# Optimization experiments

Measured on AMD Instinct MI355X. Metric: run time of the kernel, lower is better.

Reference implementation:

```python
import jax, jax.numpy as jnp
import numpy as np

N, E = 50000, 800000
NODE_IN, EDGE_IN = 32, 16
EMB, GEMB = 128, 128
H, C, L, B = 4, 32, 2, 8   # heads, per-head dim, layers, graphs
GAT_IN = NODE_IN + EMB      # skip_conn=True
NEG_SLOPE = 0.2
EPS = 1e-5


def layernorm(x, g, b):
    m = jnp.mean(x, -1, keepdims=True)
    v = jnp.mean((x - m) ** 2, -1, keepdims=True)
    return (x - m) / jnp.sqrt(v + EPS) * g + b


def setup_inputs() -> dict:
    key = jax.random.key(0)
    ks = jax.random.split(key, 24)
    s = 0.05
    return {
        "x": jax.random.normal(ks[0], (N, NODE_IN), jnp.float32),
        "edge_attr": jax.random.normal(ks[1], (E, EDGE_IN), jnp.float32),
        "W_in": jax.random.normal(ks[2], (NODE_IN, EMB), jnp.float32) * s,
        "b_in": jnp.zeros((EMB,), jnp.float32),
        "W_src": jax.random.normal(ks[3], (L, GAT_IN, H * C), jnp.float32) * s,
        "W_edge": jax.random.normal(ks[4], (L, EDGE_IN, H * C), jnp.float32) * s,
        "att_src": jax.random.normal(ks[5], (L, H, C), jnp.float32) * s,
        "att_dst": jax.random.normal(ks[6], (L, H, C), jnp.float32) * s,
        "att_edge": jax.random.normal(ks[7], (L, H, C), jnp.float32) * s,
        "gat_bias": jnp.zeros((L, H * C), jnp.float32),
        "ln_gamma": jnp.ones((L, EMB), jnp.float32),
        "ln_beta": jnp.zeros((L, EMB), jnp.float32),
        "W_out": jax.random.normal(ks[8], (EMB, EMB), jnp.float32) * s,
        "b_out": jnp.zeros((EMB,), jnp.float32),
        "ln_out_gamma": jnp.ones((EMB,), jnp.float32),
        "ln_out_beta": jnp.zeros((EMB,), jnp.float32),
        "W_g": jax.random.normal(ks[9], (EMB, GEMB), jnp.float32) * s,
        "b_g": jnp.zeros((GEMB,), jnp.float32),
        "g_gamma": jnp.ones((GEMB,), jnp.float32),
        "g_beta": jnp.zeros((GEMB,), jnp.float32),
        "edge_index": jax.random.randint(ks[10], (2, E), 0, N, jnp.int32),
        "batch": jnp.sort(jax.random.randint(ks[11], (N,), 0, B, jnp.int32)),
    }


def reference(x, edge_attr, W_in, b_in, W_src, W_edge, att_src, att_dst, att_edge,
              gat_bias, ln_gamma, ln_beta, W_out, b_out, ln_out_gamma, ln_out_beta,
              W_g, b_g, g_gamma, g_beta, edge_index, batch):
    # PyG GATConv adds self-loops with edge_attr fill_value='mean'
    loop = jnp.arange(N, dtype=edge_index.dtype)
    src = jnp.concatenate([edge_index[0], loop])   # [E2]
    dst = jnp.concatenate([edge_index[1], loop])   # [E2]
    ea = jnp.concatenate([edge_attr, jnp.broadcast_to(edge_attr.mean(0), (N, EDGE_IN))], 0)

    h = jax.nn.relu(x @ W_in + b_in)  # [N, EMB]
    for l in range(L):
        inp = jnp.concatenate([x, h], -1)                   # skip connection [N, GAT_IN]
        xs = (inp @ W_src[l]).reshape(N, H, C)              # projected nodes
        a_s = jnp.einsum('nhc,hc->nh', xs, att_src[l])
        a_d = jnp.einsum('nhc,hc->nh', xs, att_dst[l])
        ee = (ea @ W_edge[l]).reshape(-1, H, C)             # [E2, H, C]
        a_e = jnp.einsum('ehc,hc->eh', ee, att_edge[l])
        alpha = jax.nn.leaky_relu(a_s[src] + a_d[dst] + a_e, NEG_SLOPE)  # [E2, H]
        # segment softmax over incoming edges of each destination node
        amax = jax.ops.segment_max(alpha, dst, num_segments=N)
        ex = jnp.exp(alpha - amax[dst])
        denom = jax.ops.segment_sum(ex, dst, num_segments=N)
        w = ex / (denom[dst] + 1e-16)
        msg = xs[src] * w[:, :, None]                        # [E2, H, C]
        out = jax.ops.segment_sum(msg, dst, num_segments=N).reshape(N, H * C) + gat_bias[l]
        h = jax.nn.elu(layernorm(out, ln_gamma[l], ln_beta[l]))

    g = layernorm(jax.nn.relu(h @ W_g + b_g), g_gamma, g_beta)
    gsum = jax.ops.segment_sum(g, batch, num_segments=B)
    cnt = jax.ops.segment_sum(jnp.ones((N, 1), g.dtype), batch, num_segments=B)
    graph_embeddings = gsum / jnp.maximum(cnt, 1.0)

    node_embeddings = layernorm(jax.nn.relu(h @ W_out + b_out), ln_out_gamma, ln_out_beta)
    return node_embeddings, graph_embeddings
```

## Files before the change

### kernel.cpp

```cpp
#include <hip/hip_runtime.h>

#define N_NODES 50000
#define N_EDGES 800000
#define E2      850000
#define NODE_IN 32
#define EDGE_IN 16
#define EMB     128
#define GAT_IN  160
#define NLAYER  2
#define NGRAPH  8
#define NBLK    196
#define NB32    1563
#define NB64    782
#define EB      3321

#define GWT_SRC0 0
#define GWT_SRC1 20480
#define GWT_OUT  40960
#define GWT_G    57344
#define GWT_TOT  73728

typedef short bf16x8 __attribute__((ext_vector_type(8)));
typedef float f32x4 __attribute__((ext_vector_type(4)));

__device__ __forceinline__ unsigned int f2bf(float f) {
    unsigned int u = __float_as_uint(f);
    return (u + 0x7FFFu + ((u >> 16) & 1u)) >> 16;
}
__device__ __forceinline__ float bf2f(unsigned int h) {
    return __uint_as_float(h << 16);
}
__device__ __forceinline__ unsigned int pack2bf(float a, float b) {
    return f2bf(a) | (f2bf(b) << 16);
}

__global__ void zero_kernel(float* __restrict__ p, int n) {
    int i = blockIdx.x * blockDim.x + threadIdx.x;
    int stride = gridDim.x * blockDim.x;
    for (; i < n; i += stride) p[i] = 0.f;
}

__global__ __launch_bounds__(256) void mega_kernel(
    const int* __restrict__ edge_index, const float* __restrict__ edge_attr,
    const float* __restrict__ x, const float* __restrict__ W_in,
    const float* __restrict__ b_in,
    const float* __restrict__ Wsrc, const float* __restrict__ Wout,
    const float* __restrict__ Wg,
    int* __restrict__ cnt8, int* __restrict__ rank, float* __restrict__ meta,
    unsigned int* __restrict__ h_bf, unsigned int* __restrict__ x_bf,
    unsigned short* __restrict__ gwt) {
    __shared__ float smem[32 * NODE_IN];
    int b = blockIdx.x, t = threadIdx.x;

    if (b < EB) {
        int e = b * 256 + t;
        if (e < E2) {
            int dst = (e < N_EDGES) ? edge_index[N_EDGES + e] : (e - N_EDGES);
            int shard = b & 7;
            rank[e] = atomicAdd(&cnt8[shard * N_NODES + dst], 1);
        }
        if (b < 512) {
            if (t < 16) smem[t] = 0.f;
            __syncthreads();
            int gid = b * 256 + t;
            int q = gid & 3;
            const float4* ea4 = (const float4*)edge_attr;
            float4 s = make_float4(0.f, 0.f, 0.f, 0.f);
            for (int j = gid; j < N_EDGES * 4; j += 512 * 256) {
                float4 v = ea4[j];
                s.x += v.x; s.y += v.y; s.z += v.z; s.w += v.w;
            }
            atomicAdd(&smem[q * 4 + 0], s.x);
            atomicAdd(&smem[q * 4 + 1], s.y);
            atomicAdd(&smem[q * 4 + 2], s.z);
            atomicAdd(&smem[q * 4 + 3], s.w);
            __syncthreads();
            if (t < 16) atomicAdd(&meta[t], smem[t]);
        }
    } else if (b < EB + NB32) {
        float (*inp)[NODE_IN] = (float (*)[NODE_IN])smem;
        int n0 = (b - EB) * 32;
        for (int i = t; i < 32 * NODE_IN; i += 256) {
            int r = i >> 5, c = i & 31;
            int n = min(n0 + r, N_NODES - 1);
            inp[r][c] = x[(size_t)n * NODE_IN + c];
        }
        __syncthreads();
        for (int i = t; i < 32 * 16; i += 256) {
            int r = i >> 4, c = i & 15;
            int n = n0 + r;
            if (n < N_NODES) x_bf[(size_t)n * 16 + c] = pack2bf(inp[r][2 * c], inp[r][2 * c + 1]);
        }
        int wave = t >> 6, lane = t & 63;
        int c0 = lane * 2, c1 = c0 + 1;
        const float2* W2 = (const float2*)W_in;
        float acc[8][2];
#pragma unroll
        for (int j = 0; j < 8; j++) { acc[j][0] = b_in[c0]; acc[j][1] = b_in[c1]; }
#pragma unroll 2
        for (int k4 = 0; k4 < NODE_IN / 4; k4++) {
            float4 v[8];
#pragma unroll
            for (int j = 0; j < 8; j++) v[j] = *(const float4*)&inp[wave * 8 + j][k4 * 4];
#pragma unroll
            for (int kk = 0; kk < 4; kk++) {
                float2 w = W2[(k4 * 4 + kk) * 64 + lane];
#pragma unroll
                for (int j = 0; j < 8; j++) {
                    float vv = (&v[j].x)[kk];
                    acc[j][0] += vv * w.x;
                    acc[j][1] += vv * w.y;
                }
            }
        }
#pragma unroll
        for (int j = 0; j < 8; j++) {
            int n = n0 + wave * 8 + j;
            if (n < N_NODES)
                h_bf[(size_t)n * 64 + lane] = pack2bf(fmaxf(acc[j][0], 0.f), fmaxf(acc[j][1], 0.f));
        }
    } else {
        int g = (b - EB - NB32) * 256 + t;
        const float* Wm;
        int base, gg;
        if (g < 5120) {
            int l = g / 2560;
            gg = g - l * 2560;
            Wm = Wsrc + (size_t)l * GAT_IN * EMB;
            base = l * 20480;
        } else if (g < 7168) {
            gg = g - 5120;
            Wm = Wout;
            base = GWT_OUT;
        } else {
            gg = g - 7168;
            Wm = Wg;
            base = GWT_G;
        }
        int lane = gg & 63, tmp = gg >> 6;
        int nt = tmp & 7, kc = tmp >> 3;
        int quad = lane >> 4, l16 = lane & 15;
        int col = nt * 16 + l16, k0 = kc * 32 + quad * 8;
        unsigned int u[4];
#pragma unroll
        for (int j = 0; j < 4; j++)
            u[j] = pack2bf(Wm[(size_t)(k0 + 2 * j) * EMB + col],
                           Wm[(size_t)(k0 + 2 * j + 1) * EMB + col]);
        *(uint4*)(gwt + base + (size_t)gg * 8) = make_uint4(u[0], u[1], u[2], u[3]);
    }
}

__global__ __launch_bounds__(256) void scan1_kernel(const int* __restrict__ cnt8,
                                                    int* __restrict__ bsum) {
    __shared__ int sm[256];
    int t = threadIdx.x;
    int i = blockIdx.x * 256 + t;
    int tot = 0;
    if (i < N_NODES) {
#pragma unroll
        for (int s = 0; s < 8; s++) tot += cnt8[s * N_NODES + i];
    }
    sm[t] = tot;
    __syncthreads();
#pragma unroll
    for (int d = 128; d >= 1; d >>= 1) {
        if (t < d) sm[t] += sm[t + d];
        __syncthreads();
    }
    if (t == 0) bsum[blockIdx.x] = sm[0];
}

__global__ __launch_bounds__(256) void scan2_prep_kernel(const int* __restrict__ bsum,
                                                         int* __restrict__ bbase,
                                                         const float* __restrict__ W_edge,
                                                         const float* __restrict__ att_edge,
                                                         float* __restrict__ meta) {
    __shared__ int sm[256];
    int t = threadIdx.x;
    int v = (t < NBLK) ? bsum[t] : 0;
    sm[t] = v;
    __syncthreads();
#pragma unroll
    for (int d = 1; d < 256; d <<= 1) {
        int u = (t >= d) ? sm[t - d] : 0;
        __syncthreads();
        sm[t] += u;
        __syncthreads();
    }
    if (t < NBLK) bbase[t] = sm[t] - v;

    if (t < EDGE_IN) meta[t] = meta[t] * (1.0f / (float)N_EDGES);
    __syncthreads();
    if (t < 128) {
        int l = t >> 6, k = (t >> 2) & 15, h = t & 3;
        const float* w = W_edge + ((size_t)l * EDGE_IN + k) * EMB + h * 32;
        const float* a = att_edge + (size_t)l * EMB + h * 32;
        float acc = 0.f;
#pragma unroll
        for (int c = 0; c < 32; c++) acc += w[c] * a[c];
        meta[16 + (l * 16 + k) * 4 + h] = acc;
    }
    __syncthreads();
    if (t < 8) {
        int l = t >> 2, h = t & 3;
        float acc = 0.f;
#pragma unroll
        for (int k = 0; k < EDGE_IN; k++) acc += meta[k] * meta[16 + (l * 16 + k) * 4 + h];
        meta[144 + t] = acc;
    }
}

__global__ __launch_bounds__(256) void scan3_kernel(const int* __restrict__ bbase,
                                                    const int* __restrict__ cnt8,
                                                    int* __restrict__ off,
                                                    int* __restrict__ shard_base) {
    __shared__ int sm[256];
    int t = threadIdx.x;
    int i = blockIdx.x * 256 + t;
    int c[8] = {0, 0, 0, 0, 0, 0, 0, 0};
    int tot = 0;
    if (i < N_NODES) {
#pragma unroll
        for (int s = 0; s < 8; s++) {
            c[s] = cnt8[s * N_NODES + i];
            tot += c[s];
        }
    }
    sm[t] = tot;
    __syncthreads();
#pragma unroll
    for (int d = 1; d < 256; d <<= 1) {
        int u = (t >= d) ? sm[t - d] : 0;
        __syncthreads();
        sm[t] += u;
        __syncthreads();
    }
    if (i < N_NODES) {
        int base = bbase[blockIdx.x] + sm[t] - tot;
        off[i] = base;
        int4 sb0, sb1;
        sb0.x = base;           base += c[0];
        sb0.y = base;           base += c[1];
        sb0.z = base;           base += c[2];
        sb0.w = base;           base += c[3];
        sb1.x = base;           base += c[4];
        sb1.y = base;           base += c[5];
        sb1.z = base;           base += c[6];
        sb1.w = base;
        *(int4*)(shard_base + (size_t)i * 8) = sb0;
        *(int4*)(shard_base + (size_t)i * 8 + 4) = sb1;
        if (i == N_NODES - 1) off[N_NODES] = E2;
    }
}

__global__ __launch_bounds__(256) void fill_perm_kernel(const int* __restrict__ edge_index,
                                                        const int* __restrict__ rank,
                                                        const int* __restrict__ shard_base,
                                                        int* __restrict__ perm) {
    int e = blockIdx.x * 256 + threadIdx.x;
    if (e >= E2) return;
    int src, dst;
    if (e < N_EDGES) {
        src = edge_index[e];
        dst = edge_index[N_EDGES + e];
    } else {
        src = dst = e - N_EDGES;
    }
    int shard = (e >> 8) & 7;
    int pos = shard_base[(size_t)dst * 8 + shard] + rank[e];
    ((int2*)perm)[pos] = make_int2(src, e);
}

__global__ __launch_bounds__(256) void compute_ae_kernel(const int* __restrict__ perm,
                                                         const float* __restrict__ edge_attr,
                                                         const float* __restrict__ meta,
                                                         int* __restrict__ csr_src,
                                                         float* __restrict__ csr_ae0,
                                                         float* __restrict__ csr_ae1) {
    __shared__ float Ml[128];
    __shared__ float loop_ae[8];
    int t = threadIdx.x;
    if (t < 128) Ml[t] = meta[16 + t];
    if (t < 8) loop_ae[t] = meta[144 + t];
    __syncthreads();
    int p = blockIdx.x * 256 + t;
    if (p >= E2) return;
    int2 pe = ((const int2*)perm)[p];
    int src = pe.x, e = pe.y;
    csr_src[p] = src;
    float ae[2][4];
    if (e < N_EDGES) {
        const float4* r4 = (const float4*)(edge_attr + (size_t)e * EDGE_IN);
#pragma unroll
        for (int l = 0; l < 2; l++)
#pragma unroll
            for (int hh = 0; hh < 4; hh++) ae[l][hh] = 0.f;
#pragma unroll
        for (int q = 0; q < 4; q++) {
            float4 v = r4[q];
#pragma unroll
            for (int l = 0; l < 2; l++) {
                const float* M = Ml + l * 64;
#pragma unroll
                for (int hh = 0; hh < 4; hh++) {
                    ae[l][hh] += v.x * M[(4 * q + 0) * 4 + hh] + v.y * M[(4 * q + 1) * 4 + hh] +
                                 v.z * M[(4 * q + 2) * 4 + hh] + v.w * M[(4 * q + 3) * 4 + hh];
                }
            }
        }
    } else {
#pragma unroll
        for (int l = 0; l < 2; l++)
#pragma unroll
            for (int hh = 0; hh < 4; hh++) ae[l][hh] = loop_ae[l * 4 + hh];
    }
    *(float4*)(csr_ae0 + (size_t)p * 4) = make_float4(ae[0][0], ae[0][1], ae[0][2], ae[0][3]);
    *(float4*)(csr_ae1 + (size_t)p * 4) = make_float4(ae[1][0], ae[1][1], ae[1][2], ae[1][3]);
}

template <int K, int MODE>
__global__ __launch_bounds__(256) void dense_mfma_kernel(
    const unsigned int* __restrict__ xbf, const unsigned int* __restrict__ hbf,
    const unsigned short* __restrict__ gwt, const float* __restrict__ bias,
    const float* __restrict__ v1, const float* __restrict__ v2,
    const int* __restrict__ batch,
    unsigned int* __restrict__ xs_out, float* __restrict__ a_s, float* __restrict__ a_d,
    float* __restrict__ out_nodes, float* __restrict__ gsum, float* __restrict__ gcnt) {
    constexpr int CLS = 132;
    __shared__ __align__(16) float cl[64 * CLS];
    __shared__ float red[(MODE != 0) ? 64 : 1][8];
    __shared__ float locw[(MODE == 2) ? 4 : 1][2][EMB];
    __shared__ int bids[(MODE == 2) ? 64 : 1];

    int t = threadIdx.x;
    int n0 = blockIdx.x * 64;
    if (MODE == 2 && t < 64) bids[t] = batch[min(n0 + t, N_NODES - 1)];

    int wave = t >> 6, lane = t & 63;
    int quad = lane >> 4, l16 = lane & 15;
    int arow = min(n0 + wave * 16 + l16, N_NODES - 1);
    const bf16x8* B = (const bf16x8*)gwt;
    f32x4 acc[8];
#pragma unroll
    for (int i = 0; i < 8; i++) acc[i] = (f32x4){0.f, 0.f, 0.f, 0.f};
#pragma unroll
    for (int kc = 0; kc < K / 32; kc++) {
        bf16x8 af;
        if (MODE == 0 && kc == 0) {
            af = *(const bf16x8*)(xbf + (size_t)arow * 16 + quad * 4);
        } else {
            int hk = ((MODE == 0) ? (kc - 1) : kc) * 16;
            af = *(const bf16x8*)(hbf + (size_t)arow * 64 + hk + quad * 4);
        }
#pragma unroll
        for (int nt = 0; nt < 8; nt++) {
            bf16x8 bfv = B[(kc * 8 + nt) * 64 + lane];
            acc[nt] = __builtin_amdgcn_mfma_f32_16x16x32_bf16(af, bfv, acc[nt], 0, 0, 0);
        }
    }
#pragma unroll
    for (int nt = 0; nt < 8; nt++) {
#pragma unroll
        for (int i = 0; i < 4; i++) {
            int r = wave * 16 + quad * 4 + i;
            cl[r * CLS + nt * 16 + l16] = acc[nt][i];
        }
    }
    __syncthreads();

    int p = t & 3, r = t >> 2;
    int n = n0 + r;
    const float4* c4 = (const float4*)(cl + r * CLS + p * 32);

    if (MODE == 0) {
        const float4* s4 = (const float4*)(v1 + p * 32);
        const float4* d4 = (const float4*)(v2 + p * 32);
        if (n < N_NODES) {
            float s_ = 0.f, d_ = 0.f;
#pragma unroll
            for (int i = 0; i < 8; i++) {
                float4 cv = c4[i], sv = s4[i], dv = d4[i];
                s_ += cv.x * sv.x + cv.y * sv.y + cv.z * sv.z + cv.w * sv.w;
                d_ += cv.x * dv.x + cv.y * dv.y + cv.z * dv.z + cv.w * dv.w;
                uint2 pk = make_uint2(pack2bf(cv.x, cv.y), pack2bf(cv.z, cv.w));
                *(uint2*)(xs_out + (size_t)n * 64 + p * 16 + 2 * i) = pk;
            }
            a_s[(size_t)n * 4 + p] = s_;
            a_d[(size_t)n * 4 + p] = d_;
        }
    } else {
        const float4* b4 = (const float4*)(bias + p * 32);
        float vals[32];
        float s_ = 0.f, q_ = 0.f;
#pragma unroll
        for (int i = 0; i < 8; i++) {
            float4 cv = c4[i], bv = b4[i];
            float w0 = fmaxf(cv.x + bv.x, 0.f), w1 = fmaxf(cv.y + bv.y, 0.f);
            float w2 = fmaxf(cv.z + bv.z, 0.f), w3 = fmaxf(cv.w + bv.w, 0.f);
            vals[4 * i] = w0; vals[4 * i + 1] = w1; vals[4 * i + 2] = w2; vals[4 * i + 3] = w3;
            s_ += w0 + w1 + w2 + w3;
            q_ += w0 * w0 + w1 * w1 + w2 * w2 + w3 * w3;
        }
        red[r][p] = s_;
        red[r][4 + p] = q_;
        __syncthreads();
        float sm = red[r][0] + red[r][1] + red[r][2] + red[r][3];
        float sq = red[r][4] + red[r][5] + red[r][6] + red[r][7];
        float mean = sm * (1.f / EMB);
        float var = sq * (1.f / EMB) - mean * mean;
        float rstd = rsqrtf(var + 1e-5f);
        const float4* g4 = (const float4*)(v1 + p * 32);
        const float4* be4 = (const float4*)(v2 + p * 32);
#pragma unroll
        for (int i = 0; i < 8; i++) {
            float4 gv = g4[i], bv = be4[i];
            vals[4 * i]     = (vals[4 * i]     - mean) * rstd * gv.x + bv.x;
            vals[4 * i + 1] = (vals[4 * i + 1] - mean) * rstd * gv.y + bv.y;
            vals[4 * i + 2] = (vals[4 * i + 2] - mean) * rstd * gv.z + bv.z;
            vals[4 * i + 3] = (vals[4 * i + 3] - mean) * rstd * gv.w + bv.w;
        }
        if (MODE == 1) {
            if (n < N_NODES) {
                float* op = out_nodes + (size_t)n * EMB + p * 32;
#pragma unroll
                for (int i = 0; i < 8; i++)
                    *(float4*)(op + 4 * i) = make_float4(vals[4 * i], vals[4 * i + 1],
                                                         vals[4 * i + 2], vals[4 * i + 3]);
            }
        } else {
            int nvalid = min(64, N_NODES - n0);
            int bmin = bids[0], bmax = bids[nvalid - 1];
            int bid = bids[r];
            bool inA = (bid == bmin) && (n < N_NODES);
            bool inB = (bid == bmax) && (bmax != bmin) && (n < N_NODES);
            if (n < N_NODES && bid != bmin && bid != bmax) {
#pragma unroll
                for (int i = 0; i < 32; i++)
                    atomicAdd(&gsum[(size_t)bid * EMB + p * 32 + i], vals[i]);
            }
#pragma unroll
            for (int g = 0; g < 2; g++) {
                bool m = g ? inB : inA;
#pragma unroll
                for (int i = 0; i < 32; i++) {
                    float v = m ? vals[i] : 0.f;
                    v += __shfl_xor(v, 4, 64);
                    v += __shfl_xor(v, 8, 64);
                    v += __shfl_xor(v, 16, 64);
                    v += __shfl_xor(v, 32, 64);
                    if ((lane >> 2) == 0) locw[wave][g][(lane & 3) * 32 + i] = v;
                }
            }
            __syncthreads();
            if (t < 128) {
                float sA = locw[0][0][t] + locw[1][0][t] + locw[2][0][t] + locw[3][0][t];
                atomicAdd(&gsum[(size_t)bmin * EMB + t], sA);
                if (bmax != bmin) {
                    float sB = locw[0][1][t] + locw[1][1][t] + locw[2][1][t] + locw[3][1][t];
                    atomicAdd(&gsum[(size_t)bmax * EMB + t], sB);
                }
            } else if (t == 255) {
                int cA = 0, cB = 0;
                for (int rr = 0; rr < nvalid; rr++) {
                    int bb = bids[rr];
                    if (bb == bmin) cA++;
                    else if (bb == bmax) cB++;
                    else atomicAdd(&gcnt[bb], 1.f);
                }
                atomicAdd(&gcnt[bmin], (float)cA);
                if (bmax != bmin && cB > 0) atomicAdd(&gcnt[bmax], (float)cB);
            }
        }
    }
}

__global__ __launch_bounds__(256) void gat_gather_kernel(const int* __restrict__ off,
                                                         const int* __restrict__ csr_src,
                                                         const float* __restrict__ csr_ae,
                                                         const unsigned int* __restrict__ xs,
                                                         const float* __restrict__ a_s,
                                                         const float* __restrict__ a_d,
                                                         const float* __restrict__ bias_l,
                                                         const float* __restrict__ gamma_l,
                                                         const float* __restrict__ beta_l,
                                                         unsigned int* __restrict__ h_bf) {
    int t = threadIdx.x, wave = t >> 6, lane = t & 63;
    int n = blockIdx.x * 4 + wave;
    int g = lane >> 4, l16 = lane & 15;
    int h = l16 >> 2;
    float ad = a_d[(size_t)n * 4 + h];
    int p0 = __builtin_amdgcn_readfirstlane(off[n]);
    int p1 = __builtin_amdgcn_readfirstlane(off[n + 1]);
    int plast = p1 - 1;
    float den = 0.f;
    float acc[8];
#pragma unroll
    for (int j = 0; j < 8; j++) acc[j] = 0.f;

    for (int pb = p0; pb < p1; pb += 8) {
        int pA = pb + g, pB = pb + 4 + g;
        int iA = min(pA, plast), iB = min(pB, plast);
        int sA = csr_src[iA], sB = csr_src[iB];
        float aeA = csr_ae[(size_t)iA * 4 + h];
        float aeB = csr_ae[(size_t)iB * 4 + h];
        float asA = a_s[(size_t)sA * 4 + h];
        float asB = a_s[(size_t)sB * 4 + h];
        uint4 xA = *(const uint4*)(xs + (size_t)sA * 64 + l16 * 4);
        uint4 xB = *(const uint4*)(xs + (size_t)sB * 64 + l16 * 4);
        float alA = asA + ad + aeA;
        alA = alA > 0.f ? alA : 0.2f * alA;
        float exA = (pA <= plast) ? __expf(alA) : 0.f;
        float alB = asB + ad + aeB;
        alB = alB > 0.f ? alB : 0.2f * alB;
        float exB = (pB <= plast) ? __expf(alB) : 0.f;
        den += exA + exB;
        unsigned int u;
        u = xA.x; acc[0] += exA * bf2f(u & 0xFFFFu); acc[1] += exA * bf2f(u >> 16);
        u = xA.y; acc[2] += exA * bf2f(u & 0xFFFFu); acc[3] += exA * bf2f(u >> 16);
        u = xA.z; acc[4] += exA * bf2f(u & 0xFFFFu); acc[5] += exA * bf2f(u >> 16);
        u = xA.w; acc[6] += exA * bf2f(u & 0xFFFFu); acc[7] += exA * bf2f(u >> 16);
        u = xB.x; acc[0] += exB * bf2f(u & 0xFFFFu); acc[1] += exB * bf2f(u >> 16);
        u = xB.y; acc[2] += exB * bf2f(u & 0xFFFFu); acc[3] += exB * bf2f(u >> 16);
        u = xB.z; acc[4] += exB * bf2f(u & 0xFFFFu); acc[5] += exB * bf2f(u >> 16);
        u = xB.w; acc[6] += exB * bf2f(u & 0xFFFFu); acc[7] += exB * bf2f(u >> 16);
    }
#pragma unroll
    for (int j = 0; j < 8; j++) {
        acc[j] += __shfl_xor(acc[j], 16, 64);
        acc[j] += __shfl_xor(acc[j], 32, 64);
    }
    den += __shfl_xor(den, 16, 64);
    den += __shfl_xor(den, 32, 64);

    float dinv = 1.0f / (den + 1e-16f);
    int c0 = l16 * 8;
    const float4* b4 = (const float4*)(bias_l + c0);
    float4 bv0 = b4[0], bv1 = b4[1];
    float v[8];
    v[0] = acc[0] * dinv + bv0.x; v[1] = acc[1] * dinv + bv0.y;
    v[2] = acc[2] * dinv + bv0.z; v[3] = acc[3] * dinv + bv0.w;
    v[4] = acc[4] * dinv + bv1.x; v[5] = acc[5] * dinv + bv1.y;
    v[6] = acc[6] * dinv + bv1.z; v[7] = acc[7] * dinv + bv1.w;
    float sm = 0.f, sq = 0.f;
#pragma unroll
    for (int j = 0; j < 8; j++) { sm += v[j]; sq += v[j] * v[j]; }
#pragma unroll
    for (int o = 1; o <= 8; o <<= 1) {
        sm += __shfl_xor(sm, o, 64);
        sq += __shfl_xor(sq, o, 64);
    }
    float mean = sm * (1.f / EMB);
    float var = sq * (1.f / EMB) - mean * mean;
    float rstd = rsqrtf(var + 1e-5f);
    const float4* g4 = (const float4*)(gamma_l + c0);
    const float4* be4 = (const float4*)(beta_l + c0);
    float4 gv0 = g4[0], gv1 = g4[1], bev0 = be4[0], bev1 = be4[1];
    float y[8];
    y[0] = (v[0] - mean) * rstd * gv0.x + bev0.x;
    y[1] = (v[1] - mean) * rstd * gv0.y + bev0.y;
    y[2] = (v[2] - mean) * rstd * gv0.z + bev0.z;
    y[3] = (v[3] - mean) * rstd * gv0.w + bev0.w;
    y[4] = (v[4] - mean) * rstd * gv1.x + bev1.x;
    y[5] = (v[5] - mean) * rstd * gv1.y + bev1.y;
    y[6] = (v[6] - mean) * rstd * gv1.z + bev1.z;
    y[7] = (v[7] - mean) * rstd * gv1.w + bev1.w;
#pragma unroll
    for (int j = 0; j < 8; j++) y[j] = y[j] > 0.f ? y[j] : __expf(y[j]) - 1.f;
    if (g == 0) {
        uint4 o4;
        o4.x = pack2bf(y[0], y[1]);
        o4.y = pack2bf(y[2], y[3]);
        o4.z = pack2bf(y[4], y[5]);
        o4.w = pack2bf(y[6], y[7]);
        *(uint4*)(h_bf + (size_t)n * 64 + l16 * 4) = o4;
    }
}

__global__ void graph_out_kernel(const float* __restrict__ gsum, const float* __restrict__ gcnt,
                                 float* __restrict__ out) {
    int i = blockIdx.x * blockDim.x + threadIdx.x;
    if (i >= NGRAPH * EMB) return;
    int b = i >> 7;
    float c = fmaxf(gcnt[b], 1.f);
    out[(size_t)N_NODES * EMB + i] = gsum[i] / c;
}

extern "C" void kernel_launch(void* const* d_in, const int* in_sizes, int n_in,
                              void* d_out, int out_size, void* d_ws, size_t ws_size,
                              hipStream_t stream) {
    (void)in_sizes; (void)n_in; (void)out_size; (void)ws_size;
    const float* x         = (const float*)d_in[0];
    const float* edge_attr = (const float*)d_in[1];
    const float* W_in      = (const float*)d_in[2];
    const float* b_in      = (const float*)d_in[3];
    const float* W_src     = (const float*)d_in[4];
    const float* W_edge    = (const float*)d_in[5];
    const float* att_src   = (const float*)d_in[6];
    const float* att_dst   = (const float*)d_in[7];
    const float* att_edge  = (const float*)d_in[8];
    const float* gat_bias  = (const float*)d_in[9];
    const float* ln_gamma  = (const float*)d_in[10];
    const float* ln_beta   = (const float*)d_in[11];
    const float* W_out     = (const float*)d_in[12];
    const float* b_out     = (const float*)d_in[13];
    const float* ln_og     = (const float*)d_in[14];
    const float* ln_ob     = (const float*)d_in[15];
    const float* W_g       = (const float*)d_in[16];
    const float* b_g       = (const float*)d_in[17];
    const float* g_gamma   = (const float*)d_in[18];
    const float* g_beta    = (const float*)d_in[19];
    const int* edge_index  = (const int*)d_in[20];
    const int* batch       = (const int*)d_in[21];
    float* out = (float*)d_out;

    float* ws              = (float*)d_ws;
    unsigned int* h_bf     = (unsigned int*)ws;
    unsigned int* xs       = h_bf + (size_t)N_NODES * 64;
    unsigned int* x_bf     = xs + (size_t)N_NODES * 64;
    float* a_s             = (float*)(x_bf + (size_t)N_NODES * 16);
    float* a_d             = a_s + (size_t)N_NODES * 4;
    float* csr_ae          = a_d + (size_t)N_NODES * 4;
    unsigned short* gwt    = (unsigned short*)(csr_ae + (size_t)2 * E2 * 4);
    float* meta            = (float*)(gwt + GWT_TOT);
    float* gsum            = meta + 152;
    float* gcnt            = gsum + NGRAPH * EMB;
    int*   cnt8            = (int*)(gcnt + NGRAPH);
    int*   off             = cnt8 + 8 * N_NODES;
    int*   shard_base      = off + N_NODES + 1;
    int*   rank            = shard_base + 8 * N_NODES;
    int*   csr_src         = rank + E2;
    int*   bsum            = csr_src + E2;
    int*   bbase           = bsum + NBLK;
    int*   perm            = (int*)xs;

    zero_kernel<<<256, 256, 0, stream>>>(meta, 152 + NGRAPH * EMB + NGRAPH + 8 * N_NODES);
    mega_kernel<<<EB + NB32 + 36, 256, 0, stream>>>(
        edge_index, edge_attr, x, W_in, b_in, W_src, W_out, W_g,
        cnt8, rank, meta, h_bf, x_bf, gwt);

    scan1_kernel<<<NBLK, 256, 0, stream>>>(cnt8, bsum);
    scan2_prep_kernel<<<1, 256, 0, stream>>>(bsum, bbase, W_edge, att_edge, meta);
    scan3_kernel<<<NBLK, 256, 0, stream>>>(bbase, cnt8, off, shard_base);
    fill_perm_kernel<<<EB, 256, 0, stream>>>(edge_index, rank, shard_base, perm);
    compute_ae_kernel<<<EB, 256, 0, stream>>>(perm, edge_attr, meta,
                                              csr_src, csr_ae, csr_ae + (size_t)E2 * 4);

    for (int l = 0; l < NLAYER; l++) {
        dense_mfma_kernel<GAT_IN, 0><<<NB64, 256, 0, stream>>>(
            x_bf, h_bf, gwt + (l ? GWT_SRC1 : GWT_SRC0), nullptr,
            att_src + (size_t)l * EMB, att_dst + (size_t)l * EMB, nullptr,
            xs, a_s, a_d, nullptr, nullptr, nullptr);
        gat_gather_kernel<<<N_NODES / 4, 256, 0, stream>>>(
            off, csr_src, csr_ae + (size_t)l * E2 * 4, xs, a_s, a_d,
            gat_bias + (size_t)l * EMB, ln_gamma + (size_t)l * EMB,
            ln_beta + (size_t)l * EMB, h_bf);
    }

    dense_mfma_kernel<EMB, 1><<<NB64, 256, 0, stream>>>(
        nullptr, h_bf, gwt + GWT_OUT, b_out, ln_og, ln_ob, nullptr,
        nullptr, nullptr, nullptr, out, nullptr, nullptr);
    dense_mfma_kernel<EMB, 2><<<NB64, 256, 0, stream>>>(
        nullptr, h_bf, gwt + GWT_G, b_g, g_gamma, g_beta, batch,
        nullptr, nullptr, nullptr, nullptr, gsum, gcnt);
    graph_out_kernel<<<4, 256, 0, stream>>>(gsum, gcnt, out);
}
```

Measured before the change: 421.8 us.

## Replace sharded atomic CSR build with two-level bucket counting sort

Replaces the CSR construction, which used per-node sharded global atomic counters, a three-pass scan and a rank-based scatter, with a two-level counting sort. Edges are first histogrammed into 98 buckets of 512 destinations per 4096-edge chunk using shared-memory atomics, then scattered into bucket order. Each bucket is then sorted locally in shared memory to produce the offsets and the permutation. This removes the large zeroing of 400K counters and the contended global atomics, but adds an extra pass over the edge records. Only 98 blocks run the local sort, which limits parallelism, and the ordering within each node may differ from before.

```diff
diff --git a/kernel.cpp b/kernel.cpp
--- a/kernel.cpp
+++ b/kernel.cpp
@@ -9,10 +9,13 @@
 #define GAT_IN  160
 #define NLAYER  2
 #define NGRAPH  8
-#define NBLK    196
 #define NB32    1563
 #define NB64    782
 #define EB      3321
+
+#define NBUCK   98
+#define CHUNK   4096
+#define NCHUNK  208
 
 #define GWT_SRC0 0
 #define GWT_SRC1 20480
@@ -46,40 +49,47 @@
     const float* __restrict__ b_in,
     const float* __restrict__ Wsrc, const float* __restrict__ Wout,
     const float* __restrict__ Wg,
-    int* __restrict__ cnt8, int* __restrict__ rank, float* __restrict__ meta,
+    int* __restrict__ hist, float* __restrict__ meta,
     unsigned int* __restrict__ h_bf, unsigned int* __restrict__ x_bf,
     unsigned short* __restrict__ gwt) {
     __shared__ float smem[32 * NODE_IN];
     int b = blockIdx.x, t = threadIdx.x;
 
-    if (b < EB) {
-        int e = b * 256 + t;
-        if (e < E2) {
-            int dst = (e < N_EDGES) ? edge_index[N_EDGES + e] : (e - N_EDGES);
-            int shard = b & 7;
-            rank[e] = atomicAdd(&cnt8[shard * N_NODES + dst], 1);
-        }
-        if (b < 512) {
-            if (t < 16) smem[t] = 0.f;
-            __syncthreads();
-            int gid = b * 256 + t;
-            int q = gid & 3;
-            const float4* ea4 = (const float4*)edge_attr;
-            float4 s = make_float4(0.f, 0.f, 0.f, 0.f);
-            for (int j = gid; j < N_EDGES * 4; j += 512 * 256) {
-                float4 v = ea4[j];
-                s.x += v.x; s.y += v.y; s.z += v.z; s.w += v.w;
-            }
-            atomicAdd(&smem[q * 4 + 0], s.x);
-            atomicAdd(&smem[q * 4 + 1], s.y);
-            atomicAdd(&smem[q * 4 + 2], s.z);
-            atomicAdd(&smem[q * 4 + 3], s.w);
-            __syncthreads();
-            if (t < 16) atomicAdd(&meta[t], smem[t]);
-        }
-    } else if (b < EB + NB32) {
+    if (b < NCHUNK) {
+        int* lh = (int*)smem;
+        if (t < NBUCK) lh[t] = 0;
+        __syncthreads();
+        int c0 = b * CHUNK;
+#pragma unroll
+        for (int i = 0; i < CHUNK / 256; i++) {
+            int e = c0 + i * 256 + t;
+            if (e < E2) {
+                int dst = (e < N_EDGES) ? edge_index[N_EDGES + e] : (e - N_EDGES);
+                atomicAdd(&lh[dst >> 9], 1);
+            }
+        }
+        __syncthreads();
+        if (t < NBUCK) hist[t * NCHUNK + b] = lh[t];
+    } else if (b < NCHUNK + 512) {
+        if (t < 16) smem[t] = 0.f;
+        __syncthreads();
+        int gid = (b - NCHUNK) * 256 + t;
+        int q = gid & 3;
+        const float4* ea4 = (const float4*)edge_attr;
+        float4 s = make_float4(0.f, 0.f, 0.f, 0.f);
+        for (int j = gid; j < N_EDGES * 4; j += 512 * 256) {
+            float4 v = ea4[j];
+            s.x += v.x; s.y += v.y; s.z += v.z; s.w += v.w;
+        }
+        atomicAdd(&smem[q * 4 + 0], s.x);
+        atomicAdd(&smem[q * 4 + 1], s.y);
+        atomicAdd(&smem[q * 4 + 2], s.z);
+        atomicAdd(&smem[q * 4 + 3], s.w);
+        __syncthreads();
+        if (t < 16) atomicAdd(&meta[t], smem[t]);
+    } else if (b < NCHUNK + 512 + NB32) {
         float (*inp)[NODE_IN] = (float (*)[NODE_IN])smem;
-        int n0 = (b - EB) * 32;
+        int n0 = (b - NCHUNK - 512) * 32;
         for (int i = t; i < 32 * NODE_IN; i += 256) {
             int r = i >> 5, c = i & 31;
             int n = min(n0 + r, N_NODES - 1);
@@ -120,7 +130,7 @@
                 h_bf[(size_t)n * 64 + lane] = pack2bf(fmaxf(acc[j][0], 0.f), fmaxf(acc[j][1], 0.f));
         }
     } else {
-        int g = (b - EB - NB32) * 256 + t;
+        int g = (b - NCHUNK - 512 - NB32) * 256 + t;
         const float* Wm;
         int base, gg;
         if (g < 5120) {
@@ -150,34 +160,32 @@
     }
 }
 
-__global__ __launch_bounds__(256) void scan1_kernel(const int* __restrict__ cnt8,
-                                                    int* __restrict__ bsum) {
+__global__ __launch_bounds__(256) void bucket_scan_kernel(int* __restrict__ hist,
+                                                          int* __restrict__ btot) {
+    __shared__ int sm[256];
+    int k = blockIdx.x, t = threadIdx.x;
+    int v = (t < NCHUNK) ? hist[k * NCHUNK + t] : 0;
+    sm[t] = v;
+    __syncthreads();
+#pragma unroll
+    for (int d = 1; d < 256; d <<= 1) {
+        int u = (t >= d) ? sm[t - d] : 0;
+        __syncthreads();
+        sm[t] += u;
+        __syncthreads();
+    }
+    if (t < NCHUNK) hist[k * NCHUNK + t] = sm[t] - v;
+    if (t == 255) btot[k] = sm[255];
+}
+
+__global__ __launch_bounds__(256) void base_prep_kernel(const int* __restrict__ btot,
+                                                        int* __restrict__ bucket_base,
+                                                        const float* __restrict__ W_edge,
+                                                        const float* __restrict__ att_edge,
+                                                        float* __restrict__ meta) {
     __shared__ int sm[256];
     int t = threadIdx.x;
-    int i = blockIdx.x * 256 + t;
-    int tot = 0;
-    if (i < N_NODES) {
-#pragma unroll
-        for (int s = 0; s < 8; s++) tot += cnt8[s * N_NODES + i];
-    }
-    sm[t] = tot;
-    __syncthreads();
-#pragma unroll
-    for (int d = 128; d >= 1; d >>= 1) {
-        if (t < d) sm[t] += sm[t + d];
-        __syncthreads();
-    }
-    if (t == 0) bsum[blockIdx.x] = sm[0];
-}
-
-__global__ __launch_bounds__(256) void scan2_prep_kernel(const int* __restrict__ bsum,
-                                                         int* __restrict__ bbase,
-                                                         const float* __restrict__ W_edge,
-                                                         const float* __restrict__ att_edge,
-                                                         float* __restrict__ meta) {
-    __shared__ int sm[256];
-    int t = threadIdx.x;
-    int v = (t < NBLK) ? bsum[t] : 0;
+    int v = (t < NBUCK) ? btot[t] : 0;
     sm[t] = v;
     __syncthreads();
 #pragma unroll
@@ -187,7 +195,8 @@
         sm[t] += u;
         __syncthreads();
     }
-    if (t < NBLK) bbase[t] = sm[t] - v;
+    if (t < NBUCK) bucket_base[t] = sm[t] - v;
+    if (t == NBUCK - 1) bucket_base[NBUCK] = sm[t];
 
     if (t < EDGE_IN) meta[t] = meta[t] * (1.0f / (float)N_EDGES);
     __syncthreads();
@@ -210,68 +219,72 @@
     }
 }
 
-__global__ __launch_bounds__(256) void scan3_kernel(const int* __restrict__ bbase,
-                                                    const int* __restrict__ cnt8,
-                                                    int* __restrict__ off,
-                                                    int* __restrict__ shard_base) {
-    __shared__ int sm[256];
-    int t = threadIdx.x;
-    int i = blockIdx.x * 256 + t;
-    int c[8] = {0, 0, 0, 0, 0, 0, 0, 0};
-    int tot = 0;
-    if (i < N_NODES) {
-#pragma unroll
-        for (int s = 0; s < 8; s++) {
-            c[s] = cnt8[s * N_NODES + i];
-            tot += c[s];
-        }
-    }
-    sm[t] = tot;
-    __syncthreads();
-#pragma unroll
-    for (int d = 1; d < 256; d <<= 1) {
+__global__ __launch_bounds__(256) void scatter_bucket_kernel(const int* __restrict__ edge_index,
+                                                             const int* __restrict__ hist,
+                                                             const int* __restrict__ bucket_base,
+                                                             int2* __restrict__ brec) {
+    __shared__ int cur[NBUCK];
+    int b = blockIdx.x, t = threadIdx.x;
+    if (t < NBUCK) cur[t] = bucket_base[t] + hist[t * NCHUNK + b];
+    __syncthreads();
+    int c0 = b * CHUNK;
+#pragma unroll
+    for (int i = 0; i < CHUNK / 256; i++) {
+        int e = c0 + i * 256 + t;
+        if (e < E2) {
+            int src, dst;
+            if (e < N_EDGES) {
+                src = edge_index[e];
+                dst = edge_index[N_EDGES + e];
+            } else {
+                src = dst = e - N_EDGES;
+            }
+            int pos = atomicAdd(&cur[dst >> 9], 1);
+            brec[pos] = make_int2(src | ((dst & 511) << 16), e);
+        }
+    }
+}
+
+__global__ __launch_bounds__(512) void local_sort_kernel(const int* __restrict__ bucket_base,
+                                                         const int2* __restrict__ brec,
+                                                         int* __restrict__ off,
+                                                         int2* __restrict__ perm) {
+    __shared__ int lh[512];
+    __shared__ int sm[512];
+    int k = blockIdx.x, t = threadIdx.x;
+    int base = bucket_base[k], end = bucket_base[k + 1], cnt = end - base;
+    lh[t] = 0;
+    __syncthreads();
+    for (int i = t; i < cnt; i += 512) {
+        int2 r = brec[base + i];
+        atomicAdd(&lh[(r.x >> 16) & 511], 1);
+    }
+    __syncthreads();
+    int v = lh[t];
+    sm[t] = v;
+    __syncthreads();
+#pragma unroll
+    for (int d = 1; d < 512; d <<= 1) {
         int u = (t >= d) ? sm[t - d] : 0;
         __syncthreads();
         sm[t] += u;
         __syncthreads();
     }
-    if (i < N_NODES) {
-        int base = bbase[blockIdx.x] + sm[t] - tot;
-        off[i] = base;
-        int4 sb0, sb1;
-        sb0.x = base;           base += c[0];
-        sb0.y = base;           base += c[1];
-        sb0.z = base;           base += c[2];
-        sb0.w = base;           base += c[3];
-        sb1.x = base;           base += c[4];
-        sb1.y = base;           base += c[5];
-        sb1.z = base;           base += c[6];
-        sb1.w = base;
-        *(int4*)(shard_base + (size_t)i * 8) = sb0;
-        *(int4*)(shard_base + (size_t)i * 8 + 4) = sb1;
-        if (i == N_NODES - 1) off[N_NODES] = E2;
-    }
-}
-
-__global__ __launch_bounds__(256) void fill_perm_kernel(const int* __restrict__ edge_index,
-                                                        const int* __restrict__ rank,
-                                                        const int* __restrict__ shard_base,
-                                                        int* __restrict__ perm) {
-    int e = blockIdx.x * 256 + threadIdx.x;
-    if (e >= E2) return;
-    int src, dst;
-    if (e < N_EDGES) {
-        src = edge_index[e];
-        dst = edge_index[N_EDGES + e];
-    } else {
-        src = dst = e - N_EDGES;
-    }
-    int shard = (e >> 8) & 7;
-    int pos = shard_base[(size_t)dst * 8 + shard] + rank[e];
-    ((int2*)perm)[pos] = make_int2(src, e);
-}
-
-__global__ __launch_bounds__(256) void compute_ae_kernel(const int* __restrict__ perm,
+    int excl = sm[t] - v;
+    int dst = (k << 9) + t;
+    if (dst < N_NODES) off[dst] = base + excl;
+    if (k == NBUCK - 1 && t == 0) off[N_NODES] = E2;
+    lh[t] = excl;
+    __syncthreads();
+    for (int i = t; i < cnt; i += 512) {
+        int2 r = brec[base + i];
+        int dl = (r.x >> 16) & 511;
+        int p = atomicAdd(&lh[dl], 1);
+        perm[base + p] = make_int2(r.x & 0xFFFF, r.y);
+    }
+}
+
+__global__ __launch_bounds__(256) void compute_ae_kernel(const int2* __restrict__ perm,
                                                          const float* __restrict__ edge_attr,
                                                          const float* __restrict__ meta,
                                                          int* __restrict__ csr_src,
@@ -285,7 +298,7 @@
     __syncthreads();
     int p = blockIdx.x * 256 + t;
     if (p >= E2) return;
-    int2 pe = ((const int2*)perm)[p];
+    int2 pe = perm[p];
     int src = pe.x, e = pe.y;
     csr_src[p] = src;
     float ae[2][4];
@@ -624,24 +637,23 @@
     float* meta            = (float*)(gwt + GWT_TOT);
     float* gsum            = meta + 152;
     float* gcnt            = gsum + NGRAPH * EMB;
-    int*   cnt8            = (int*)(gcnt + NGRAPH);
-    int*   off             = cnt8 + 8 * N_NODES;
-    int*   shard_base      = off + N_NODES + 1;
-    int*   rank            = shard_base + 8 * N_NODES;
-    int*   csr_src         = rank + E2;
-    int*   bsum            = csr_src + E2;
-    int*   bbase           = bsum + NBLK;
-    int*   perm            = (int*)xs;
-
-    zero_kernel<<<256, 256, 0, stream>>>(meta, 152 + NGRAPH * EMB + NGRAPH + 8 * N_NODES);
-    mega_kernel<<<EB + NB32 + 36, 256, 0, stream>>>(
+    int*   off             = (int*)(gcnt + NGRAPH);
+    int*   csr_src         = off + N_NODES + 2;
+    int2*  brec            = (int2*)(csr_src + E2);
+    int*   hist            = (int*)(brec + E2);
+    int*   btot            = hist + NBUCK * NCHUNK;
+    int*   bucket_base     = btot + NBUCK;
+    int2*  perm            = (int2*)xs;
+
+    zero_kernel<<<8, 256, 0, stream>>>(meta, 152 + NGRAPH * EMB + NGRAPH);
+    mega_kernel<<<NCHUNK + 512 + NB32 + 36, 256, 0, stream>>>(
         edge_index, edge_attr, x, W_in, b_in, W_src, W_out, W_g,
-        cnt8, rank, meta, h_bf, x_bf, gwt);
-
-    scan1_kernel<<<NBLK, 256, 0, stream>>>(cnt8, bsum);
-    scan2_prep_kernel<<<1, 256, 0, stream>>>(bsum, bbase, W_edge, att_edge, meta);
-    scan3_kernel<<<NBLK, 256, 0, stream>>>(bbase, cnt8, off, shard_base);
-    fill_perm_kernel<<<EB, 256, 0, stream>>>(edge_index, rank, shard_base, perm);
+        hist, meta, h_bf, x_bf, gwt);
+
+    bucket_scan_kernel<<<NBUCK, 256, 0, stream>>>(hist, btot);
+    base_prep_kernel<<<1, 256, 0, stream>>>(btot, bucket_base, W_edge, att_edge, meta);
+    scatter_bucket_kernel<<<NCHUNK, 256, 0, stream>>>(edge_index, hist, bucket_base, brec);
+    local_sort_kernel<<<NBUCK, 512, 0, stream>>>(bucket_base, brec, off, perm);
     compute_ae_kernel<<<EB, 256, 0, stream>>>(perm, edge_attr, meta,
                                               csr_src, csr_ae, csr_ae + (size_t)E2 * 4);
 
```

After: 399.1 us. 5.4% less time.
